# Kernel optimization log

Measured on AMD Instinct MI355X. Metric: run time of the kernel, lower is better.

Reference implementation:

```python
import jax, jax.numpy as jnp
import numpy as np

B, S, D = 2, 2048, 2048
H, KVH, HD = 16, 4, 128
REP = H // KVH  # 4
THETA = 10000.0


def setup_inputs() -> dict:
    key = jax.random.key(0)
    ks = jax.random.split(key, 5)
    scale = 0.02
    x = jax.random.normal(ks[0], (B, S, D), dtype=jnp.float32)
    Wq = jax.random.normal(ks[1], (D, H * HD), dtype=jnp.float32) * scale
    Wk = jax.random.normal(ks[2], (D, KVH * HD), dtype=jnp.float32) * scale
    Wv = jax.random.normal(ks[3], (D, KVH * HD), dtype=jnp.float32) * scale
    Wo = jax.random.normal(ks[4], (H * HD, D), dtype=jnp.float32) * scale
    return {"x": x, "Wq": Wq, "Wk": Wk, "Wv": Wv, "Wo": Wo}


def _rope_cos_sin(seq_len, dtype):
    # HF-style rotary embedding: inv_freq over even dims, duplicated halves
    inv_freq = 1.0 / (THETA ** (jnp.arange(0, HD, 2, dtype=jnp.float32) / HD))
    pos = jnp.arange(seq_len, dtype=jnp.float32)
    ang = pos[:, None] * inv_freq[None, :]          # [S, HD/2]
    emb = jnp.concatenate([ang, ang], axis=-1)       # [S, HD]
    return jnp.cos(emb).astype(dtype), jnp.sin(emb).astype(dtype)


def _rotate_half(t):
    t1, t2 = jnp.split(t, 2, axis=-1)
    return jnp.concatenate([-t2, t1], axis=-1)


def reference(x, Wq, Wk, Wv, Wo):
    bsz, seq_len, _ = x.shape
    q = (x @ Wq).reshape(bsz, seq_len, H, HD).transpose(0, 2, 1, 3)    # [B,H,S,HD]
    k = (x @ Wk).reshape(bsz, seq_len, KVH, HD).transpose(0, 2, 1, 3)  # [B,KVH,S,HD]
    v = (x @ Wv).reshape(bsz, seq_len, KVH, HD).transpose(0, 2, 1, 3)
    cos, sin = _rope_cos_sin(seq_len, q.dtype)       # [S,HD]
    cos = cos[None, None, :, :]
    sin = sin[None, None, :, :]
    q = q * cos + _rotate_half(q) * sin
    k = k * cos + _rotate_half(k) * sin
    # repeat_interleave KV heads to match Q heads
    k = jnp.repeat(k, REP, axis=1)                   # [B,H,S,HD]
    v = jnp.repeat(v, REP, axis=1)
    scores = jnp.einsum('bhqd,bhkd->bhqk', q, k) / jnp.sqrt(jnp.float32(HD)).astype(q.dtype)
    i = jnp.arange(seq_len)
    causal = jnp.where(i[None, :] > i[:, None], jnp.float32(-jnp.inf), 0.0).astype(scores.dtype)
    scores = scores + causal[None, None, :, :]
    probs = jax.nn.softmax(scores.astype(jnp.float32), axis=-1).astype(q.dtype)
    out = jnp.einsum('bhqk,bhkd->bhqd', probs, v)    # [B,H,S,HD]
    out = out.transpose(0, 2, 1, 3).reshape(bsz, seq_len, H * HD)
    return out @ Wo
```

## Files before the change

kernel.cpp:

```cpp
#include <hip/hip_runtime.h>
#include <math.h>

#define B_   2
#define S_   2048
#define D_   2048
#define H_   16
#define KVH_ 4
#define HD_  128
#define REP_ 4

typedef __attribute__((ext_vector_type(8))) short bf16x8;
typedef __attribute__((ext_vector_type(4))) short bf16x4;
typedef __attribute__((ext_vector_type(4))) float f32x4;

#define QSCALE_LOG2E 0.1275266977097153f

__device__ __forceinline__ unsigned short f2bf(float x) {
    union { float f; unsigned u; } v; v.f = x;
    unsigned r = v.u + 0x7FFF + ((v.u >> 16) & 1);
    return (unsigned short)(r >> 16);
}

__device__ __forceinline__ unsigned short f2bf_fast(float x) {
    union { float f; unsigned u; } v; v.f = x;
    return (unsigned short)((v.u + 0x8000) >> 16);
}

__device__ __forceinline__ void gl_lds16(const unsigned short* g, unsigned short* l) {
    __builtin_amdgcn_global_load_lds(
        (const __attribute__((address_space(1))) unsigned int*)g,
        (__attribute__((address_space(3))) unsigned int*)l,
        16, 0, 0);
}

__global__ void cast_bf16(const float* __restrict__ src,
                          unsigned short* __restrict__ dst, int n4)
{
    int i = blockIdx.x * 256 + threadIdx.x;
    if (i >= n4) return;
    float4 v = *(const float4*)&src[(size_t)i * 4];
    bf16x4 o;
    o[0] = (short)f2bf(v.x); o[1] = (short)f2bf(v.y);
    o[2] = (short)f2bf(v.z); o[3] = (short)f2bf(v.w);
    *(bf16x4*)&dst[(size_t)i * 4] = o;
}

__global__ __launch_bounds__(256) void cast_transpose_all(
    const float* __restrict__ Wq, const float* __restrict__ Wk,
    const float* __restrict__ Wv, const float* __restrict__ Wo,
    unsigned short* __restrict__ Wqt, unsigned short* __restrict__ Wkt,
    unsigned short* __restrict__ Wvt, unsigned short* __restrict__ Wot)
{
    __shared__ float T[32][33];
    const int y = blockIdx.y;
    const float* src; unsigned short* dst; int C, bj;
    if (y < 64)      { src = Wq; dst = Wqt; C = 2048; bj = y; }
    else if (y < 80) { src = Wk; dst = Wkt; C = 512;  bj = y - 64; }
    else if (y < 96) { src = Wv; dst = Wvt; C = 512;  bj = y - 80; }
    else             { src = Wo; dst = Wot; C = 2048; bj = y - 96; }

    const int bi = blockIdx.x;
    const int t  = threadIdx.x;
    const int r  = t >> 3, cq = (t & 7) * 4;

    float4 v = *(const float4*)&src[(size_t)(bi * 32 + r) * C + bj * 32 + cq];
    T[r][cq + 0] = v.x; T[r][cq + 1] = v.y;
    T[r][cq + 2] = v.z; T[r][cq + 3] = v.w;
    __syncthreads();

    bf16x4 o;
    o[0] = (short)f2bf(T[cq + 0][r]);
    o[1] = (short)f2bf(T[cq + 1][r]);
    o[2] = (short)f2bf(T[cq + 2][r]);
    o[3] = (short)f2bf(T[cq + 3][r]);
    *(bf16x4*)&dst[(size_t)(bj * 32 + r) * 2048 + bi * 32 + cq] = o;
}

__global__ __launch_bounds__(256) void qkv_mfma(
    const unsigned short* __restrict__ Ah,
    const unsigned short* __restrict__ Wqt,
    const unsigned short* __restrict__ Wkt,
    const unsigned short* __restrict__ Wvt,
    unsigned short* __restrict__ Qh, unsigned short* __restrict__ Kh,
    unsigned short* __restrict__ Vt)
{
    __shared__ __align__(16) char smem[34816];
    unsigned short* As = (unsigned short*)smem;
    unsigned short* Bs = (unsigned short*)(smem + 8192);
    unsigned short* Ts = (unsigned short*)smem;

    const int bm = blockIdx.x, bn = blockIdx.y;
    const int m0 = bm * 128, n0 = bn * 128;
    const int tid  = threadIdx.x;
    const int w    = tid >> 6;
    const int lane = tid & 63;
    const int lo16 = lane & 15, quad = lane >> 4;
    const int wm   = w >> 1, wn = w & 1;
    const int cmap[4] = { wn * 2, wn * 2 + 1, wn * 2 + 4, wn * 2 + 5 };

    const unsigned short* Bt;
    if (n0 < 2048)      Bt = Wqt + (size_t)n0 * 2048;
    else if (n0 < 2560) Bt = Wkt + (size_t)(n0 - 2048) * 2048;
    else                Bt = Wvt + (size_t)(n0 - 2560) * 2048;

    const unsigned short* Ag = Ah + (size_t)m0 * 2048;

    f32x4 acc[4][4];
    #pragma unroll
    for (int im = 0; im < 4; ++im)
        #pragma unroll
        for (int jn = 0; jn < 4; ++jn) acc[im][jn] = (f32x4){0.f, 0.f, 0.f, 0.f};

    const int srow = w * 32 + (lane >> 2);
    const int scol = (lane & 3) * 8;

    for (int kt = 0; kt < 2048; kt += 32) {
        __syncthreads();
        gl_lds16(Ag + (size_t)(srow     ) * 2048 + kt + scol, As + (w * 32     ) * 32);
        gl_lds16(Ag + (size_t)(srow + 16) * 2048 + kt + scol, As + (w * 32 + 16) * 32);
        gl_lds16(Bt + (size_t)(srow     ) * 2048 + kt + scol, Bs + (w * 32     ) * 32);
        gl_lds16(Bt + (size_t)(srow + 16) * 2048 + kt + scol, Bs + (w * 32 + 16) * 32);
        __syncthreads();

        bf16x8 af[4], bf[4];
        #pragma unroll
        for (int im = 0; im < 4; ++im)
            af[im] = *(const bf16x8*)&As[(wm * 64 + im * 16 + lo16) * 32 + quad * 8];
        #pragma unroll
        for (int jn = 0; jn < 4; ++jn)
            bf[jn] = *(const bf16x8*)&Bs[(cmap[jn] * 16 + lo16) * 32 + quad * 8];
        #pragma unroll
        for (int im = 0; im < 4; ++im)
            #pragma unroll
            for (int jn = 0; jn < 4; ++jn)
                acc[im][jn] = __builtin_amdgcn_mfma_f32_16x16x32_bf16(
                    af[im], bf[jn], acc[im][jn], 0, 0, 0);
    }
    __syncthreads();

    const int bb = m0 >> 11;
    const int s0 = m0 & 2047;

    if (n0 < 2560) {
        const bool isQ = (n0 < 2048);
        const int h = isQ ? (n0 >> 7) : ((n0 - 2048) >> 7);
        const float post = isQ ? QSCALE_LOG2E : 1.0f;
        unsigned short* dstbase = isQ
            ? Qh + (((size_t)bb * H_   + h) * S_) * HD_
            : Kh + (((size_t)bb * KVH_ + h) * S_) * HD_;
        float inv[2];
        #pragma unroll
        for (int jn = 0; jn < 2; ++jn)
            inv[jn] = exp2f(-(float)((wn * 2 + jn) * 16 + lo16) * 0.20761871093344086f);
        #pragma unroll
        for (int im = 0; im < 4; ++im) {
            #pragma unroll
            for (int r = 0; r < 4; ++r) {
                int s = s0 + wm * 64 + im * 16 + quad * 4 + r;
                unsigned short* drow = dstbase + (size_t)s * HD_;
                #pragma unroll
                for (int jn = 0; jn < 2; ++jn) {
                    int d = (wn * 2 + jn) * 16 + lo16;
                    float ang = (float)s * inv[jn];
                    float sn, c;
                    sincosf(ang, &sn, &c);
                    float lo = acc[im][jn][r], hi = acc[im][jn + 2][r];
                    drow[d]      = f2bf((lo * c - hi * sn) * post);
                    drow[d + 64] = f2bf((hi * c + lo * sn) * post);
                }
            }
        }
    } else {
        const int g = (n0 - 2560) >> 7;
        #pragma unroll
        for (int im = 0; im < 4; ++im)
            #pragma unroll
            for (int jn = 0; jn < 4; ++jn)
                #pragma unroll
                for (int r = 0; r < 4; ++r)
                    Ts[(size_t)(cmap[jn] * 16 + lo16) * 136
                       + (wm * 64 + im * 16 + quad * 4 + r)] = f2bf(acc[im][jn][r]);
        __syncthreads();
        unsigned short* dstbase = Vt + (((size_t)bb * KVH_ + g) * HD_) * S_ + s0;
        #pragma unroll
        for (int it = 0; it < 8; ++it) {
            int u = it * 256 + tid;
            int d = u >> 4, ch = (u & 15) * 8;
            *(bf16x8*)(dstbase + (size_t)d * S_ + ch) = *(const bf16x8*)&Ts[(size_t)d * 136 + ch];
        }
    }
}

__global__ __launch_bounds__(256, 2) void flash_attn_mfma(
    const unsigned short* __restrict__ Qh,
    const unsigned short* __restrict__ Kh,
    const unsigned short* __restrict__ Vt,
    unsigned short* __restrict__ attb)
{
    const int bh   = blockIdx.x;
    const int yy   = blockIdx.y;
    const int qt   = (yy < 8) ? (15 - yy) : (yy - 8);
    const int b    = bh >> 4, h = bh & 15;
    const int g    = h >> 2;
    const int tid  = threadIdx.x;
    const int w    = tid >> 6;
    const int lane = tid & 63;
    const int lo16 = lane & 15;
    const int quad = lane >> 4;

    const unsigned short* Qb = Qh + (((size_t)b * H_   + h) * S_) * HD_;
    const unsigned short* Kb = Kh + (((size_t)b * KVH_ + g) * S_) * HD_;
    const unsigned short* Vb = Vt + (((size_t)b * KVH_ + g) * HD_) * S_;

    __shared__ __align__(16) unsigned short Ks[64][136];
    __shared__ __align__(16) unsigned short Vs[128][72];
    __shared__ __align__(16) unsigned short Ps[4][32][72];

    const int q0 = qt * 128;
    const int qw = q0 + w * 32;

    bf16x8 qf[2][4];
    #pragma unroll
    for (int st = 0; st < 2; ++st)
        #pragma unroll
        for (int kc = 0; kc < 4; ++kc)
            qf[st][kc] = *(const bf16x8*)(Qb + (size_t)(qw + st * 16 + lo16) * HD_
                                             + kc * 32 + quad * 8);

    f32x4 o[2][8];
    #pragma unroll
    for (int st = 0; st < 2; ++st)
        #pragma unroll
        for (int n = 0; n < 8; ++n) o[st][n] = (f32x4){0.f, 0.f, 0.f, 0.f};
    float l_loc[2][4];
    #pragma unroll
    for (int st = 0; st < 2; ++st)
        #pragma unroll
        for (int r = 0; r < 4; ++r) l_loc[st][r] = 0.0f;

    const int kr = tid >> 4, kch = (tid & 15) * 8;
    const int vr = tid >> 3, vch = (tid & 7) * 8;

    bf16x8 kreg[4], vreg[4];
    #pragma unroll
    for (int i = 0; i < 4; ++i) {
        kreg[i] = *(const bf16x8*)(Kb + (size_t)(16 * i + kr) * HD_ + kch);
        vreg[i] = *(const bf16x8*)(Vb + (size_t)(32 * i + vr) * S_ + vch);
    }

    const int ktend = 2 * qt + 1;
    for (int kt = 0; kt <= ktend; ++kt) {
        const int k0 = kt * 64;
        __syncthreads();
        #pragma unroll
        for (int i = 0; i < 4; ++i) {
            *(bf16x8*)&Ks[16 * i + kr][kch] = kreg[i];
            *(bf16x8*)&Vs[32 * i + vr][vch] = vreg[i];
        }
        if (kt < ktend) {
            const int k0n = k0 + 64;
            #pragma unroll
            for (int i = 0; i < 4; ++i) {
                kreg[i] = *(const bf16x8*)(Kb + (size_t)(k0n + 16 * i + kr) * HD_ + kch);
                vreg[i] = *(const bf16x8*)(Vb + (size_t)(32 * i + vr) * S_ + k0n + vch);
            }
        }
        __syncthreads();

        if (w >= 2 || kt < ktend) {
            f32x4 sc[2][4];
            #pragma unroll
            for (int st = 0; st < 2; ++st)
                #pragma unroll
                for (int cb = 0; cb < 4; ++cb) sc[st][cb] = (f32x4){0.f, 0.f, 0.f, 0.f};
            #pragma unroll
            for (int kc = 0; kc < 4; ++kc)
                #pragma unroll
                for (int cb = 0; cb < 4; ++cb) {
                    bf16x8 kf = *(const bf16x8*)&Ks[cb * 16 + lo16][kc * 32 + quad * 8];
                    #pragma unroll
                    for (int st = 0; st < 2; ++st)
                        sc[st][cb] = __builtin_amdgcn_mfma_f32_16x16x32_bf16(
                            qf[st][kc], kf, sc[st][cb], 0, 0, 0);
                }

            const bool masked = (w < 2) ? (kt == 2 * qt) : (kt == ktend);
            if (masked) {
                #pragma unroll
                for (int st = 0; st < 2; ++st)
                    #pragma unroll
                    for (int r = 0; r < 4; ++r) {
                        const int row = qw + st * 16 + quad * 4 + r;
                        float lacc = 0.0f;
                        #pragma unroll
                        for (int cb = 0; cb < 4; ++cb) {
                            float xv = sc[st][cb][r];
                            if ((k0 + cb * 16 + lo16) > row) xv = -1e30f;
                            float p = exp2f(xv);
                            lacc += p;
                            Ps[w][st * 16 + quad * 4 + r][cb * 16 + lo16] = f2bf_fast(p);
                        }
                        l_loc[st][r] += lacc;
                    }
            } else {
                #pragma unroll
                for (int st = 0; st < 2; ++st)
                    #pragma unroll
                    for (int r = 0; r < 4; ++r) {
                        float lacc = 0.0f;
                        #pragma unroll
                        for (int cb = 0; cb < 4; ++cb) {
                            float p = exp2f(sc[st][cb][r]);
                            lacc += p;
                            Ps[w][st * 16 + quad * 4 + r][cb * 16 + lo16] = f2bf_fast(p);
                        }
                        l_loc[st][r] += lacc;
                    }
            }

            #pragma unroll
            for (int kc = 0; kc < 2; ++kc) {
                bf16x8 pf[2];
                #pragma unroll
                for (int st = 0; st < 2; ++st)
                    pf[st] = *(const bf16x8*)&Ps[w][st * 16 + lo16][kc * 32 + quad * 8];
                #pragma unroll
                for (int n = 0; n < 8; ++n) {
                    bf16x8 vf = *(const bf16x8*)&Vs[n * 16 + lo16][kc * 32 + quad * 8];
                    #pragma unroll
                    for (int st = 0; st < 2; ++st)
                        o[st][n] = __builtin_amdgcn_mfma_f32_16x16x32_bf16(
                            pf[st], vf, o[st][n], 0, 0, 0);
                }
            }
        }
    }

    #pragma unroll
    for (int st = 0; st < 2; ++st)
        #pragma unroll
        for (int r = 0; r < 4; ++r) {
            float l = l_loc[st][r];
            l += __shfl_xor(l, 1);
            l += __shfl_xor(l, 2);
            l += __shfl_xor(l, 4);
            l += __shfl_xor(l, 8);
            float invl = 1.0f / l;
            int srow = qw + st * 16 + quad * 4 + r;
            unsigned short* dst = attb + ((size_t)b * S_ + srow) * D_ + h * HD_;
            #pragma unroll
            for (int n = 0; n < 8; ++n)
                dst[n * 16 + lo16] = f2bf(o[st][n][r] * invl);
        }
}

__global__ __launch_bounds__(256) void out_mfma(
    const unsigned short* __restrict__ Ah,
    const unsigned short* __restrict__ Wot,
    float* __restrict__ C)
{
    __shared__ __align__(16) unsigned short As[128 * 32];
    __shared__ __align__(16) unsigned short Bs[128 * 32];

    const int bm = blockIdx.x, bn = blockIdx.y;
    const int m0 = bm * 128, n0 = bn * 128;
    const int tid  = threadIdx.x;
    const int w    = tid >> 6;
    const int lane = tid & 63;
    const int lo16 = lane & 15, quad = lane >> 4;
    const int wm   = w >> 1, wn = w & 1;
    const int cmap[4] = { wn * 2, wn * 2 + 1, wn * 2 + 4, wn * 2 + 5 };

    const unsigned short* Ag = Ah  + (size_t)m0 * 2048;
    const unsigned short* Bt = Wot + (size_t)n0 * 2048;

    f32x4 acc[4][4];
    #pragma unroll
    for (int im = 0; im < 4; ++im)
        #pragma unroll
        for (int jn = 0; jn < 4; ++jn) acc[im][jn] = (f32x4){0.f, 0.f, 0.f, 0.f};

    const int srow = w * 32 + (lane >> 2);
    const int scol = (lane & 3) * 8;

    for (int kt = 0; kt < 2048; kt += 32) {
        __syncthreads();
        gl_lds16(Ag + (size_t)(srow     ) * 2048 + kt + scol, As + (w * 32     ) * 32);
        gl_lds16(Ag + (size_t)(srow + 16) * 2048 + kt + scol, As + (w * 32 + 16) * 32);
        gl_lds16(Bt + (size_t)(srow     ) * 2048 + kt + scol, Bs + (w * 32     ) * 32);
        gl_lds16(Bt + (size_t)(srow + 16) * 2048 + kt + scol, Bs + (w * 32 + 16) * 32);
        __syncthreads();

        bf16x8 af[4], bf[4];
        #pragma unroll
        for (int im = 0; im < 4; ++im)
            af[im] = *(const bf16x8*)&As[(wm * 64 + im * 16 + lo16) * 32 + quad * 8];
        #pragma unroll
        for (int jn = 0; jn < 4; ++jn)
            bf[jn] = *(const bf16x8*)&Bs[(cmap[jn] * 16 + lo16) * 32 + quad * 8];
        #pragma unroll
        for (int im = 0; im < 4; ++im)
            #pragma unroll
            for (int jn = 0; jn < 4; ++jn)
                acc[im][jn] = __builtin_amdgcn_mfma_f32_16x16x32_bf16(
                    af[im], bf[jn], acc[im][jn], 0, 0, 0);
    }

    #pragma unroll
    for (int im = 0; im < 4; ++im)
        #pragma unroll
        for (int r = 0; r < 4; ++r) {
            size_t m = (size_t)(m0 + wm * 64 + im * 16 + quad * 4 + r);
            #pragma unroll
            for (int jn = 0; jn < 4; ++jn)
                C[m * 2048 + n0 + cmap[jn] * 16 + lo16] = acc[im][jn][r];
        }
}

extern "C" void kernel_launch(void* const* d_in, const int* in_sizes, int n_in,
                              void* d_out, int out_size, void* d_ws, size_t ws_size,
                              hipStream_t stream)
{
    const float* x  = (const float*)d_in[0];
    const float* Wq = (const float*)d_in[1];
    const float* Wk = (const float*)d_in[2];
    const float* Wv = (const float*)d_in[3];
    const float* Wo = (const float*)d_in[4];
    float* out = (float*)d_out;

    unsigned short* xh  = (unsigned short*)d_ws;
    unsigned short* Wqt = xh  + (size_t)4096 * 2048;
    unsigned short* Wkt = Wqt + (size_t)2048 * 2048;
    unsigned short* Wvt = Wkt + (size_t)512 * 2048;
    unsigned short* Wot = Wvt + (size_t)512 * 2048;
    unsigned short* Qh  = Wot + (size_t)2048 * 2048;
    unsigned short* Kh  = Qh  + (size_t)B_ * H_   * S_ * HD_;
    unsigned short* Vt  = Kh  + (size_t)B_ * KVH_ * S_ * HD_;
    unsigned short* attb= xh;

    cast_bf16<<<(4096 * 2048 / 4 + 255) / 256, 256, 0, stream>>>(x, xh, 4096 * 2048 / 4);
    cast_transpose_all<<<dim3(64, 160), 256, 0, stream>>>(Wq, Wk, Wv, Wo, Wqt, Wkt, Wvt, Wot);

    qkv_mfma<<<dim3(32, 24), 256, 0, stream>>>(xh, Wqt, Wkt, Wvt, Qh, Kh, Vt);

    flash_attn_mfma<<<dim3(32, 16), 256, 0, stream>>>(Qh, Kh, Vt, attb);

    out_mfma<<<dim3(32, 16), 256, 0, stream>>>(attb, Wot, out);
}
```

Measured before the change: 325.7 us.

## Rewrite QKV GEMM as 256x256-tile, 8-wave, double-buffered pipelined kernel

Replaces the 128x128, 4-wave QKV projection GEMM with a 256x256-tile, 512-thread kernel. It uses a 64-wide K step with double-buffered LDS, XOR-swizzled LDS layout and global-to-LDS loads issued ahead of the MFMA phases. Fine-grained barriers, vmcnt waits and s_setprio interleave loads with MFMA work, and a block-index swizzle improves L2 reuse. The epilogues for RoPE and the V transpose are adapted to the bigger tile, each handling two heads. This trades 128KB of LDS and high register pressure for more reuse per tile and overlapped memory traffic, but gives only 192 blocks.

New measurement: 293.6 us. 1.11x faster.

```diff
diff --git a/kernel.cpp b/kernel.cpp
--- a/kernel.cpp
+++ b/kernel.cpp
@@ -32,6 +32,12 @@
         (__attribute__((address_space(3))) unsigned int*)l,
         16, 0, 0);
 }
+
+#define PH_BAR() do { asm volatile("" ::: "memory"); \
+                      __builtin_amdgcn_s_barrier();  \
+                      asm volatile("" ::: "memory"); } while (0)
+#define VMW6 asm volatile("s_waitcnt vmcnt(6)" ::: "memory")
+#define VMW0 asm volatile("s_waitcnt vmcnt(0)" ::: "memory")
 
 __global__ void cast_bf16(const float* __restrict__ src,
                           unsigned short* __restrict__ dst, int n4)
@@ -76,7 +82,7 @@
     *(bf16x4*)&dst[(size_t)(bj * 32 + r) * 2048 + bi * 32 + cq] = o;
 }
 
-__global__ __launch_bounds__(256) void qkv_mfma(
+__global__ __launch_bounds__(512, 2) void qkv_mfma8(
     const unsigned short* __restrict__ Ah,
     const unsigned short* __restrict__ Wqt,
     const unsigned short* __restrict__ Wkt,
@@ -84,111 +90,186 @@
     unsigned short* __restrict__ Qh, unsigned short* __restrict__ Kh,
     unsigned short* __restrict__ Vt)
 {
-    __shared__ __align__(16) char smem[34816];
-    unsigned short* As = (unsigned short*)smem;
-    unsigned short* Bs = (unsigned short*)(smem + 8192);
-    unsigned short* Ts = (unsigned short*)smem;
-
-    const int bm = blockIdx.x, bn = blockIdx.y;
-    const int m0 = bm * 128, n0 = bn * 128;
+    __shared__ __align__(16) unsigned short lds[65536];
+
+    const int bid = blockIdx.x;
+    const int swz = (bid & 7) * 24 + (bid >> 3);
+    const int bm = swz / 12, bn = swz % 12;
+    const int m0 = bm * 256, n0 = bn * 256;
+
     const int tid  = threadIdx.x;
     const int w    = tid >> 6;
     const int lane = tid & 63;
     const int lo16 = lane & 15, quad = lane >> 4;
-    const int wm   = w >> 1, wn = w & 1;
-    const int cmap[4] = { wn * 2, wn * 2 + 1, wn * 2 + 4, wn * 2 + 5 };
+    const int wm   = w >> 2, wn = w & 3;
 
     const unsigned short* Bt;
     if (n0 < 2048)      Bt = Wqt + (size_t)n0 * 2048;
     else if (n0 < 2560) Bt = Wkt + (size_t)(n0 - 2048) * 2048;
     else                Bt = Wvt + (size_t)(n0 - 2560) * 2048;
-
-    const unsigned short* Ag = Ah + (size_t)m0 * 2048;
-
-    f32x4 acc[4][4];
-    #pragma unroll
-    for (int im = 0; im < 4; ++im)
-        #pragma unroll
-        for (int jn = 0; jn < 4; ++jn) acc[im][jn] = (f32x4){0.f, 0.f, 0.f, 0.f};
-
-    const int srow = w * 32 + (lane >> 2);
-    const int scol = (lane & 3) * 8;
-
-    for (int kt = 0; kt < 2048; kt += 32) {
-        __syncthreads();
-        gl_lds16(Ag + (size_t)(srow     ) * 2048 + kt + scol, As + (w * 32     ) * 32);
-        gl_lds16(Ag + (size_t)(srow + 16) * 2048 + kt + scol, As + (w * 32 + 16) * 32);
-        gl_lds16(Bt + (size_t)(srow     ) * 2048 + kt + scol, Bs + (w * 32     ) * 32);
-        gl_lds16(Bt + (size_t)(srow + 16) * 2048 + kt + scol, Bs + (w * 32 + 16) * 32);
-        __syncthreads();
-
-        bf16x8 af[4], bf[4];
-        #pragma unroll
-        for (int im = 0; im < 4; ++im)
-            af[im] = *(const bf16x8*)&As[(wm * 64 + im * 16 + lo16) * 32 + quad * 8];
-        #pragma unroll
-        for (int jn = 0; jn < 4; ++jn)
-            bf[jn] = *(const bf16x8*)&Bs[(cmap[jn] * 16 + lo16) * 32 + quad * 8];
-        #pragma unroll
-        for (int im = 0; im < 4; ++im)
-            #pragma unroll
-            for (int jn = 0; jn < 4; ++jn)
-                acc[im][jn] = __builtin_amdgcn_mfma_f32_16x16x32_bf16(
-                    af[im], bf[jn], acc[im][jn], 0, 0, 0);
+    const unsigned short* Ag   = Ah + (size_t)m0 * 2048;
+    const unsigned short* AgH1 = Ag + (size_t)128 * 2048;
+    const unsigned short* BtH1 = Bt + (size_t)128 * 2048;
+
+    const int rs   = lane >> 3;
+    const int sce  = (((lane & 7) ^ rs) << 3);
+    const int grow = w * 8 + rs;
+
+    #define STAGE(gb, k0, lb) do {                                          \
+        const unsigned short* _g = (gb) + (size_t)grow * 2048 + (k0) + sce; \
+        gl_lds16(_g,                     (lb) + w * 512);                   \
+        gl_lds16(_g + (size_t)64 * 2048, (lb) + (8 + w) * 512);             \
+    } while (0)
+
+    const int swb = (lo16 & 7) << 4;
+    const int ac0 = (quad << 4) ^ swb;
+    const int ac1 = (64 | (quad << 4)) ^ swb;
+    char* ldsb = (char*)lds;
+    const int abase = (wm * 128 + lo16) * 128;
+    const int bbase = (wn * 16 + lo16) * 128 + 32768;
+
+    f32x4 acc[8][4];
+    #pragma unroll
+    for (int mf = 0; mf < 8; ++mf)
+        #pragma unroll
+        for (int j = 0; j < 4; ++j) acc[mf][j] = (f32x4){0.f, 0.f, 0.f, 0.f};
+
+    bf16x8 a0[4][2], a1[4][2], b0[2][2], b1[2][2];
+
+    #define MM(Aa, Bb, mo, jo)                                               \
+        _Pragma("unroll") for (int mf = 0; mf < 4; ++mf)                     \
+        _Pragma("unroll") for (int j = 0; j < 2; ++j) {                      \
+            acc[(mo)+mf][(jo)+j] = __builtin_amdgcn_mfma_f32_16x16x32_bf16(  \
+                Aa[mf][0], Bb[j][0], acc[(mo)+mf][(jo)+j], 0, 0, 0);         \
+            acc[(mo)+mf][(jo)+j] = __builtin_amdgcn_mfma_f32_16x16x32_bf16(  \
+                Aa[mf][1], Bb[j][1], acc[(mo)+mf][(jo)+j], 0, 0, 0);         \
+        }
+
+    STAGE(Bt,   0,  lds + 16384);
+    STAGE(BtH1, 0,  lds + 24576);
+    STAGE(Ag,   0,  lds + 0);
+    STAGE(AgH1, 0,  lds + 8192);
+    STAGE(Bt,   64, lds + 32768 + 16384);
+    STAGE(BtH1, 64, lds + 32768 + 24576);
+    STAGE(Ag,   64, lds + 32768);
+    VMW6;
+    PH_BAR();
+
+    #define PHASES(p, t)                                                         \
+    {                              \
+        _Pragma("unroll") for (int mf = 0; mf < 4; ++mf) {                       \
+            a0[mf][0] = *(const bf16x8*)(ldsb + (p)*65536 + abase + mf*2048 + ac0); \
+            a0[mf][1] = *(const bf16x8*)(ldsb + (p)*65536 + abase + mf*2048 + ac1); \
+        }                                                                        \
+        _Pragma("unroll") for (int j = 0; j < 2; ++j) {                          \
+            b0[j][0] = *(const bf16x8*)(ldsb + (p)*65536 + bbase + j*8192 + ac0); \
+            b0[j][1] = *(const bf16x8*)(ldsb + (p)*65536 + bbase + j*8192 + ac1); \
+        }                                                                        \
+        STAGE(AgH1, ((t)+1)*64, lds + ((p)^1)*32768 + 8192);                     \
+        PH_BAR(); __builtin_amdgcn_s_setprio(1);                                 \
+        MM(a0, b0, 0, 0);                                                        \
+        __builtin_amdgcn_s_setprio(0); PH_BAR();                                 \
+                                             \
+        _Pragma("unroll") for (int j = 0; j < 2; ++j) {                          \
+            b1[j][0] = *(const bf16x8*)(ldsb + (p)*65536 + bbase + (j+2)*8192 + ac0); \
+            b1[j][1] = *(const bf16x8*)(ldsb + (p)*65536 + bbase + (j+2)*8192 + ac1); \
+        }                                                                        \
+        STAGE(Bt, ((t)+2)*64, lds + (p)*32768 + 16384);                          \
+        PH_BAR(); __builtin_amdgcn_s_setprio(1);                                 \
+        MM(a0, b1, 0, 2);                                                        \
+        __builtin_amdgcn_s_setprio(0); PH_BAR();                                 \
+                                             \
+        _Pragma("unroll") for (int mf = 0; mf < 4; ++mf) {                       \
+            a1[mf][0] = *(const bf16x8*)(ldsb + (p)*65536 + abase + (mf+4)*2048 + ac0); \
+            a1[mf][1] = *(const bf16x8*)(ldsb + (p)*65536 + abase + (mf+4)*2048 + ac1); \
+        }                                                                        \
+        STAGE(BtH1, ((t)+2)*64, lds + (p)*32768 + 24576);                        \
+        PH_BAR(); __builtin_amdgcn_s_setprio(1);                                 \
+        MM(a1, b0, 4, 0);                                                        \
+        __builtin_amdgcn_s_setprio(0); PH_BAR();                                 \
+                                  \
+        STAGE(Ag, ((t)+2)*64, lds + (p)*32768);                                  \
+        PH_BAR(); __builtin_amdgcn_s_setprio(1);                                 \
+        MM(a1, b1, 4, 2);                                                        \
+        __builtin_amdgcn_s_setprio(0);                                           \
+        VMW6;                                                                    \
+        PH_BAR();                                                                \
     }
-    __syncthreads();
+
+    for (int it = 0; it < 16; ++it) {
+        const int t = 2 * it;
+        PHASES(0, t);
+        PHASES(1, t + 1);
+    }
+
+    VMW0;
+    PH_BAR();
 
     const int bb = m0 >> 11;
-    const int s0 = m0 & 2047;
+    const int s0loc = m0 & 2047;
 
     if (n0 < 2560) {
         const bool isQ = (n0 < 2048);
-        const int h = isQ ? (n0 >> 7) : ((n0 - 2048) >> 7);
+        const int h0 = isQ ? (n0 >> 7) : ((n0 - 2048) >> 7);
         const float post = isQ ? QSCALE_LOG2E : 1.0f;
-        unsigned short* dstbase = isQ
-            ? Qh + (((size_t)bb * H_   + h) * S_) * HD_
-            : Kh + (((size_t)bb * KVH_ + h) * S_) * HD_;
-        float inv[2];
-        #pragma unroll
-        for (int jn = 0; jn < 2; ++jn)
-            inv[jn] = exp2f(-(float)((wn * 2 + jn) * 16 + lo16) * 0.20761871093344086f);
-        #pragma unroll
-        for (int im = 0; im < 4; ++im) {
+        unsigned short* db[2];
+        #pragma unroll
+        for (int hp = 0; hp < 2; ++hp)
+            db[hp] = isQ
+                ? Qh + (((size_t)bb * H_   + h0 + hp) * S_) * HD_
+                : Kh + (((size_t)bb * KVH_ + h0 + hp) * S_) * HD_;
+        const int d = wn * 16 + lo16;
+        const float inv = exp2f(-(float)d * 0.20761871093344086f);
+        #pragma unroll
+        for (int mf = 0; mf < 8; ++mf) {
             #pragma unroll
             for (int r = 0; r < 4; ++r) {
-                int s = s0 + wm * 64 + im * 16 + quad * 4 + r;
-                unsigned short* drow = dstbase + (size_t)s * HD_;
-                #pragma unroll
-                for (int jn = 0; jn < 2; ++jn) {
-                    int d = (wn * 2 + jn) * 16 + lo16;
-                    float ang = (float)s * inv[jn];
-                    float sn, c;
-                    sincosf(ang, &sn, &c);
-                    float lo = acc[im][jn][r], hi = acc[im][jn + 2][r];
+                int s = s0loc + wm * 128 + mf * 16 + quad * 4 + r;
+                float sn, c;
+                sincosf((float)s * inv, &sn, &c);
+                #pragma unroll
+                for (int hp = 0; hp < 2; ++hp) {
+                    float lo = acc[mf][2 * hp + 0][r];
+                    float hi = acc[mf][2 * hp + 1][r];
+                    unsigned short* drow = db[hp] + (size_t)s * HD_;
                     drow[d]      = f2bf((lo * c - hi * sn) * post);
                     drow[d + 64] = f2bf((hi * c + lo * sn) * post);
                 }
             }
         }
     } else {
-        const int g = (n0 - 2560) >> 7;
-        #pragma unroll
-        for (int im = 0; im < 4; ++im)
-            #pragma unroll
-            for (int jn = 0; jn < 4; ++jn)
-                #pragma unroll
-                for (int r = 0; r < 4; ++r)
-                    Ts[(size_t)(cmap[jn] * 16 + lo16) * 136
-                       + (wm * 64 + im * 16 + quad * 4 + r)] = f2bf(acc[im][jn][r]);
-        __syncthreads();
-        unsigned short* dstbase = Vt + (((size_t)bb * KVH_ + g) * HD_) * S_ + s0;
-        #pragma unroll
-        for (int it = 0; it < 8; ++it) {
-            int u = it * 256 + tid;
-            int d = u >> 4, ch = (u & 15) * 8;
-            *(bf16x8*)(dstbase + (size_t)d * S_ + ch) = *(const bf16x8*)&Ts[(size_t)d * 136 + ch];
+        const int g0 = (n0 - 2560) >> 7;
+        unsigned short* Ts = lds;
+        const int d = wn * 16 + lo16;
+        #pragma unroll
+        for (int hp = 0; hp < 2; ++hp) {
+            if (hp) PH_BAR();
+            #pragma unroll
+            for (int mf = 0; mf < 8; ++mf) {
+                int ml = wm * 128 + mf * 16 + quad * 4;
+                bf16x4 v0, v1;
+                #pragma unroll
+                for (int r = 0; r < 4; ++r) {
+                    v0[r] = (short)f2bf(acc[mf][2 * hp + 0][r]);
+                    v1[r] = (short)f2bf(acc[mf][2 * hp + 1][r]);
+                }
+                *(bf16x4*)&Ts[(size_t)d        * 264 + ml] = v0;
+                *(bf16x4*)&Ts[(size_t)(d + 64) * 264 + ml] = v1;
+            }
+            PH_BAR();
+            unsigned short* dstb = Vt + (((size_t)bb * KVH_ + g0 + hp) * HD_) * S_ + s0loc;
+            #pragma unroll
+            for (int itb = 0; itb < 8; ++itb) {
+                int dd = itb * 16 + (tid >> 5);
+                int ch = (tid & 31) * 8;
+                *(bf16x8*)(dstb + (size_t)dd * S_ + ch) =
+                    *(const bf16x8*)&Ts[(size_t)dd * 264 + ch];
+            }
         }
     }
+    #undef PHASES
+    #undef MM
+    #undef STAGE
 }
 
 __global__ __launch_bounds__(256, 2) void flash_attn_mfma(
@@ -441,7 +522,7 @@
     cast_bf16<<<(4096 * 2048 / 4 + 255) / 256, 256, 0, stream>>>(x, xh, 4096 * 2048 / 4);
     cast_transpose_all<<<dim3(64, 160), 256, 0, stream>>>(Wq, Wk, Wv, Wo, Wqt, Wkt, Wvt, Wot);
 
-    qkv_mfma<<<dim3(32, 24), 256, 0, stream>>>(xh, Wqt, Wkt, Wvt, Qh, Kh, Vt);
+    qkv_mfma8<<<192, 512, 0, stream>>>(xh, Wqt, Wkt, Wvt, Qh, Kh, Vt);
 
     flash_attn_mfma<<<dim3(32, 16), 256, 0, stream>>>(Qh, Kh, Vt, attb);
 
```
